# Kernel optimization log

Hardware: AMD Instinct MI355X
Metric: run time of the kernel (lower is better)

Reference implementation:

```python
import jax, jax.numpy as jnp
import numpy as np

B = 4096
N_ENTITY = 100000
N_USER = 10000
N_RELATION = 32
DIM = 64
N_ITER = 2
K = 16  # n_neighbors


def setup_inputs() -> dict:
    key = jax.random.key(0)
    ks = jax.random.split(key, 8)
    pairs = jax.random.randint(ks[0], (B, 2), 0, N_USER, dtype=jnp.int64 if jax.config.jax_enable_x64 else jnp.int32)
    adj_entity = jax.random.randint(ks[1], (N_ENTITY, K), 0, N_ENTITY)
    adj_relation = jax.random.randint(ks[2], (N_ENTITY, K), 0, N_RELATION)
    # xavier_uniform-style scale for embeddings
    def xavier(k, shape):
        limit = float(np.sqrt(6.0 / (shape[0] + shape[1])))
        return jax.random.uniform(k, shape, jnp.float32, -limit, limit)
    entity_emb = xavier(ks[3], (N_ENTITY, DIM))
    relation_emb = xavier(ks[4], (N_RELATION, DIM))
    user_emb = xavier(ks[5], (N_USER, DIM))
    W = xavier(ks[6], (DIM, DIM))
    b = jnp.zeros((DIM,), jnp.float32)
    return {"pairs": pairs, "adj_entity": adj_entity, "adj_relation": adj_relation,
            "entity_emb": entity_emb, "relation_emb": relation_emb,
            "user_emb": user_emb, "W": W, "b": b}


def reference(pairs, adj_entity, adj_relation, entity_emb, relation_emb, user_emb, W, b):
    n = pairs.shape[0]
    dim = entity_emb.shape[1]
    k = adj_entity.shape[1]
    users = pairs[:, 0]
    items = pairs[:, 1]

    # multi-hop neighbor expansion (mirrors get_neighbors)
    entities = [items]
    relations = []
    for i in range(N_ITER):
        entities.append(adj_entity[entities[i]].reshape(-1))
        relations.append(adj_relation[entities[i]].reshape(-1))

    u = user_emb[users]  # [B, D]
    ev = [entity_emb[entities[i]].reshape(n, -1, dim) for i in range(N_ITER + 1)]
    rv = [relation_emb[relations[i]].reshape(n, -1, dim) for i in range(N_ITER)]

    for l in range(N_ITER):
        nxt = []
        for i in range(N_ITER - l):
            r = rv[i].reshape(n, -1, k, dim)          # [B, M, K, D]
            scores = jnp.einsum('bd,bmkd->bmk', u, r) # user-relation attention
            attn = jax.nn.softmax(scores, axis=-1)[..., None]
            nbr = (attn * ev[i + 1].reshape(n, -1, k, dim)).sum(axis=-2)  # [B, M, D]
            x = ev[i].reshape(n, -1, dim) + nbr       # residual add
            h = x @ W.T + b                            # Linear(dim, dim)
            nxt.append(jnp.tanh(h) if l == N_ITER - 1 else jax.nn.relu(h))
        ev = nxt

    item_embeddings = ev[0].reshape(-1, dim)  # [B, D]
    return jax.nn.sigmoid(jnp.sum(u * item_embeddings, axis=1))
```

## Files before the change

kernel.cpp:

```cpp
#include <hip/hip_runtime.h>
#include <hip/hip_bf16.h>
#include <math.h>

#define DIM  64
#define KN   16
#define NREL 32

__device__ __forceinline__ float frcp(float x) { return __builtin_amdgcn_rcpf(x); }

__device__ __forceinline__ unsigned short f2bf(float f) {
    unsigned u = __float_as_uint(f);
    u = (u + 0x7fffu + ((u >> 16) & 1u)) >> 16;
    return (unsigned short)u;
}
__device__ __forceinline__ float bflo(unsigned v) { return __uint_as_float(v << 16); }
__device__ __forceinline__ float bfhi(unsigned v) { return __uint_as_float(v & 0xffff0000u); }

typedef __attribute__((ext_vector_type(8))) short bfrag;
typedef __attribute__((ext_vector_type(4))) float f32x4;

__global__ __launch_bounds__(256, 2) void we_kernel_mfma(
    const float* __restrict__ entity_emb,
    const float* __restrict__ W,
    const int* __restrict__ adjE,
    const int* __restrict__ adjR,
    unsigned short* __restrict__ WEb,
    int* __restrict__ adjP,
    int nRows)
{
    const int tid  = threadIdx.x;
    const int wave = tid >> 6;
    const int lane = tid & 63;
    const int c = lane & 15;
    const int g = lane >> 4;

    {
        const size_t nEntries = (size_t)nRows * KN;
        const size_t base = ((size_t)blockIdx.x * 256 + tid) * 8;
        if (base + 8 <= nEntries) {
            const int4* e4 = (const int4*)(adjE + base);
            const int4* r4 = (const int4*)(adjR + base);
            const int4 e0 = e4[0], e1v = e4[1];
            const int4 r0 = r4[0], r1v = r4[1];
            int4 p0, p1;
            p0.x = (e0.x << 5) | r0.x;  p0.y = (e0.y << 5) | r0.y;
            p0.z = (e0.z << 5) | r0.z;  p0.w = (e0.w << 5) | r0.w;
            p1.x = (e1v.x << 5) | r1v.x; p1.y = (e1v.y << 5) | r1v.y;
            p1.z = (e1v.z << 5) | r1v.z; p1.w = (e1v.w << 5) | r1v.w;
            ((int4*)(adjP + base))[0] = p0;
            ((int4*)(adjP + base))[1] = p1;
        } else if (base < nEntries) {
            for (size_t i = base; i < nEntries; ++i)
                adjP[i] = (adjE[i] << 5) | adjR[i];
        }
    }

    const int nTiles = (nRows + 15) >> 4;
    const int t0 = (blockIdx.x * 4 + wave) * 2;
    if (t0 >= nTiles) return;

    bfrag a[4][2];
    #pragma unroll
    for (int m = 0; m < 4; ++m) {
        #pragma unroll
        for (int ks = 0; ks < 2; ++ks) {
            const float4* ws = (const float4*)(W + (size_t)(16 * m + c) * DIM + 8 * g + 32 * ks);
            const float4 w0 = ws[0], w1 = ws[1];
            a[m][ks][0] = (short)f2bf(w0.x); a[m][ks][1] = (short)f2bf(w0.y);
            a[m][ks][2] = (short)f2bf(w0.z); a[m][ks][3] = (short)f2bf(w0.w);
            a[m][ks][4] = (short)f2bf(w1.x); a[m][ks][5] = (short)f2bf(w1.y);
            a[m][ks][6] = (short)f2bf(w1.z); a[m][ks][7] = (short)f2bf(w1.w);
        }
    }

    float4 pe[2][4];
    #pragma unroll
    for (int j = 0; j < 2; ++j) {
        const int t = (t0 + j < nTiles) ? (t0 + j) : 0;
        int row = 16 * t + c;
        if (row >= nRows) row = nRows - 1;
        const float4* src = (const float4*)(entity_emb + (size_t)row * DIM + 8 * g);
        pe[j][0] = src[0];
        pe[j][1] = src[1];
        pe[j][2] = src[8];
        pe[j][3] = src[9];
    }

    #pragma unroll
    for (int j = 0; j < 2; ++j) {
        const int t = t0 + j;
        if (t >= nTiles) continue;

        bfrag b0, b1;
        b0[0] = (short)f2bf(pe[j][0].x); b0[1] = (short)f2bf(pe[j][0].y);
        b0[2] = (short)f2bf(pe[j][0].z); b0[3] = (short)f2bf(pe[j][0].w);
        b0[4] = (short)f2bf(pe[j][1].x); b0[5] = (short)f2bf(pe[j][1].y);
        b0[6] = (short)f2bf(pe[j][1].z); b0[7] = (short)f2bf(pe[j][1].w);
        b1[0] = (short)f2bf(pe[j][2].x); b1[1] = (short)f2bf(pe[j][2].y);
        b1[2] = (short)f2bf(pe[j][2].z); b1[3] = (short)f2bf(pe[j][2].w);
        b1[4] = (short)f2bf(pe[j][3].x); b1[5] = (short)f2bf(pe[j][3].y);
        b1[6] = (short)f2bf(pe[j][3].z); b1[7] = (short)f2bf(pe[j][3].w);

        f32x4 acc[4];
        #pragma unroll
        for (int m = 0; m < 4; ++m) {
            f32x4 z = {0.f, 0.f, 0.f, 0.f};
            z = __builtin_amdgcn_mfma_f32_16x16x32_bf16(a[m][0], b0, z, 0, 0, 0);
            z = __builtin_amdgcn_mfma_f32_16x16x32_bf16(a[m][1], b1, z, 0, 0, 0);
            acc[m] = z;
        }

        const int erow = 16 * t + c;
        if (erow < nRows) {
            #pragma unroll
            for (int m = 0; m < 4; ++m) {
                const unsigned lo = (unsigned)f2bf(acc[m][0]) | ((unsigned)f2bf(acc[m][1]) << 16);
                const unsigned hi = (unsigned)f2bf(acc[m][2]) | ((unsigned)f2bf(acc[m][3]) << 16);
                *(uint2*)(WEb + (size_t)erow * DIM + 16 * m + 4 * g) = make_uint2(lo, hi);
            }
        }
    }
}

__global__ __launch_bounds__(256, 3) void kgcn_main(
    const int* __restrict__ pairs,
    const int* __restrict__ adjP,
    const unsigned short* __restrict__ WEb,
    const float* __restrict__ relation_emb,
    const float* __restrict__ user_emb,
    const float* __restrict__ W,
    const float* __restrict__ bias,
    float* __restrict__ out,
    int nPairs)
{
    __shared__ float ev1_s[4][KN * DIM];
    __shared__ float xb_s[4][DIM];

    const int tid  = threadIdx.x;
    const int wave = tid >> 6;
    const int lane = tid & 63;
    const int p    = blockIdx.x * 4 + wave;
    if (p >= nPairs) return;

    float* ev1 = ev1_s[wave];
    float* xb  = xb_s[wave];

    const int qq = lane >> 4;
    const int c  = lane & 15;
    const int c4 = c * 4;

    const int user = pairs[2 * p + 0];
    const int item = pairs[2 * p + 1];

    const float4 b4 = *(const float4*)(bias + c4);
    const uint2* WEq = (const uint2*)WEb;

    int rk0 = 0, e1 = 0;
    if (lane < KN) {
        const int pk0 = adjP[(size_t)item * KN + lane];
        rk0 = pk0 & 31;
        e1  = pk0 >> 5;
    }

    float4 rr[8], ur[8];
    {
        const int r = lane >> 1, hlf = lane & 1;
        const float4* rel4 = (const float4*)(relation_emb + r * DIM + hlf * 32);
        const float4* u4   = (const float4*)(user_emb + (size_t)user * DIM + hlf * 32);
        #pragma unroll
        for (int j = 0; j < 8; ++j) { rr[j] = rel4[j]; ur[j] = u4[j]; }
    }

    const uint2 itemv = WEq[(size_t)item * 16 + c];
    uint2 h0v[4];
    #pragma unroll
    for (int k = 0; k < 4; ++k) {
        const int e = __shfl(e1, qq * 4 + k);
        h0v[k] = WEq[(size_t)(unsigned)e * 16 + c];
    }
    int rkA[4], ekA[4], gsA[4];
    #pragma unroll
    for (int s = 0; s < 4; ++s) {
        gsA[s] = __shfl(e1, 4 * s + qq);
        const int pk = adjP[(size_t)(unsigned)gsA[s] * KN + c];
        rkA[s] = pk & 31;
        ekA[s] = pk >> 5;
    }

    float acc;
    {
        float a0 = 0.f, a1 = 0.f;
        #pragma unroll
        for (int j = 0; j < 8; j += 2) {
            float4 a = rr[j],     b = ur[j];
            float4 cc = rr[j+1],  d = ur[j+1];
            a0 += a.x*b.x + a.y*b.y + a.z*b.z + a.w*b.w;
            a1 += cc.x*d.x + cc.y*d.y + cc.z*d.z + cc.w*d.w;
        }
        acc = a0 + a1;
        acc += __shfl_xor(acc, 1);
    }

    uint2 svA[4];
    uint2 nvA[3][KN];
    #pragma unroll
    for (int s = 0; s < 3; ++s) {
        svA[s] = WEq[(size_t)(unsigned)gsA[s] * 16 + c];
        #pragma unroll
        for (int k = 0; k < KN; ++k) {
            const int e = __shfl(ekA[s], qq * 16 + k);
            nvA[s][k] = WEq[(size_t)(unsigned)e * 16 + c];
        }
    }
    svA[3] = WEq[(size_t)(unsigned)gsA[3] * 16 + c];

    auto softmax16 = [&](float s) -> float {
        float mx = s;
        mx = fmaxf(mx, __shfl_xor(mx, 1));
        mx = fmaxf(mx, __shfl_xor(mx, 2));
        mx = fmaxf(mx, __shfl_xor(mx, 4));
        mx = fmaxf(mx, __shfl_xor(mx, 8));
        float e = __expf(s - mx);
        float ss = e;
        ss += __shfl_xor(ss, 1);
        ss += __shfl_xor(ss, 2);
        ss += __shfl_xor(ss, 4);
        ss += __shfl_xor(ss, 8);
        return e * frcp(ss);
    };

    float wA[4];
    #pragma unroll
    for (int s = 0; s < 4; ++s) wA[s] = softmax16(__shfl(acc, rkA[s] << 1));
    const float w0 = softmax16(__shfl(acc, rk0 << 1));

    {
        float ax = b4.x + bflo(svA[0].x);
        float ay = b4.y + bfhi(svA[0].x);
        float az = b4.z + bflo(svA[0].y);
        float aw = b4.w + bfhi(svA[0].y);
        #pragma unroll
        for (int k = 0; k < KN; ++k) {
            const float w = __shfl(wA[0], qq * 16 + k);
            uint2 v = nvA[0][k];
            ax += w * bflo(v.x);
            ay += w * bfhi(v.x);
            az += w * bflo(v.y);
            aw += w * bfhi(v.y);
        }
        *(float4*)&ev1[qq * DIM + c4] =
            make_float4(fmaxf(ax, 0.f), fmaxf(ay, 0.f), fmaxf(az, 0.f), fmaxf(aw, 0.f));
    }
    uint2 nv3[KN];
    #pragma unroll
    for (int k = 0; k < KN; ++k) {
        const int e = __shfl(ekA[3], qq * 16 + k);
        nv3[k] = WEq[(size_t)(unsigned)e * 16 + c];
    }
    #pragma unroll
    for (int s = 1; s < 3; ++s) {
        float ax = b4.x + bflo(svA[s].x);
        float ay = b4.y + bfhi(svA[s].x);
        float az = b4.z + bflo(svA[s].y);
        float aw = b4.w + bfhi(svA[s].y);
        #pragma unroll
        for (int k = 0; k < KN; ++k) {
            const float w = __shfl(wA[s], qq * 16 + k);
            uint2 v = nvA[s][k];
            ax += w * bflo(v.x);
            ay += w * bfhi(v.x);
            az += w * bflo(v.y);
            aw += w * bfhi(v.y);
        }
        *(float4*)&ev1[(4 * s + qq) * DIM + c4] =
            make_float4(fmaxf(ax, 0.f), fmaxf(ay, 0.f), fmaxf(az, 0.f), fmaxf(aw, 0.f));
    }
    {
        float ax = b4.x + bflo(svA[3].x);
        float ay = b4.y + bfhi(svA[3].x);
        float az = b4.z + bflo(svA[3].y);
        float aw = b4.w + bfhi(svA[3].y);
        #pragma unroll
        for (int k = 0; k < KN; ++k) {
            const float w = __shfl(wA[3], qq * 16 + k);
            uint2 v = nv3[k];
            ax += w * bflo(v.x);
            ay += w * bfhi(v.x);
            az += w * bflo(v.y);
            aw += w * bfhi(v.y);
        }
        *(float4*)&ev1[(12 + qq) * DIM + c4] =
            make_float4(fmaxf(ax, 0.f), fmaxf(ay, 0.f), fmaxf(az, 0.f), fmaxf(aw, 0.f));
    }

    float ax = 0.f, ay = 0.f, az = 0.f, aw = 0.f;
    #pragma unroll
    for (int k = 0; k < 4; ++k) {
        const float w = __shfl(w0, qq * 4 + k);
        ax += w * bflo(h0v[k].x);
        ay += w * bfhi(h0v[k].x);
        az += w * bflo(h0v[k].y);
        aw += w * bfhi(h0v[k].y);
    }
    ax += __shfl_xor(ax, 16); ay += __shfl_xor(ay, 16);
    az += __shfl_xor(az, 16); aw += __shfl_xor(aw, 16);
    ax += __shfl_xor(ax, 32); ay += __shfl_xor(ay, 32);
    az += __shfl_xor(az, 32); aw += __shfl_xor(aw, 32);
    ax += bflo(itemv.x) + b4.x;
    ay += bfhi(itemv.x) + b4.y;
    az += bflo(itemv.y) + b4.z;
    aw += bfhi(itemv.y) + b4.w;
    const float e0x = fmaxf(ax, 0.f), e0y = fmaxf(ay, 0.f);
    const float e0z = fmaxf(az, 0.f), e0w = fmaxf(aw, 0.f);

    asm volatile("s_waitcnt lgkmcnt(0)" ::: "memory");
    float sx = 0.f, sy = 0.f, sz = 0.f, sw = 0.f;
    #pragma unroll
    for (int k = 0; k < 4; ++k) {
        const int   kg = qq * 4 + k;
        const float w  = __shfl(w0, kg);
        float4 ev = *(const float4*)&ev1[kg * DIM + c4];
        sx += w * ev.x;
        sy += w * ev.y;
        sz += w * ev.z;
        sw += w * ev.w;
    }
    sx += __shfl_xor(sx, 16); sy += __shfl_xor(sy, 16);
    sz += __shfl_xor(sz, 16); sw += __shfl_xor(sw, 16);
    sx += __shfl_xor(sx, 32); sy += __shfl_xor(sy, 32);
    sz += __shfl_xor(sz, 32); sw += __shfl_xor(sw, 32);

    asm volatile("s_waitcnt lgkmcnt(0)" ::: "memory");
    if (qq == 0)
        *(float4*)&xb[c4] = make_float4(e0x + sx, e0y + sy, e0z + sz, e0w + sw);
    asm volatile("s_waitcnt lgkmcnt(0)" ::: "memory");
    float h0 = bias[lane], h1 = 0.f, h2 = 0.f, h3 = 0.f;
    {
        const float4* Wl  = (const float4*)(W + lane * DIM);
        const float4* xv4 = (const float4*)xb;
        #pragma unroll
        for (int j = 0; j < 16; j += 4) {
            float4 w0v = Wl[j],   x0v = xv4[j];
            float4 w1v = Wl[j+1], x1v = xv4[j+1];
            float4 w2v = Wl[j+2], x2v = xv4[j+2];
            float4 w3v = Wl[j+3], x3v = xv4[j+3];
            h0 += w0v.x*x0v.x + w0v.y*x0v.y + w0v.z*x0v.z + w0v.w*x0v.w;
            h1 += w1v.x*x1v.x + w1v.y*x1v.y + w1v.z*x1v.z + w1v.w*x1v.w;
            h2 += w2v.x*x2v.x + w2v.y*x2v.y + w2v.z*x2v.z + w2v.w*x2v.w;
            h3 += w3v.x*x3v.x + w3v.y*x3v.y + w3v.z*x3v.z + w3v.w*x3v.w;
        }
    }
    const float itemf = tanhf((h0 + h1) + (h2 + h3));

    float d = user_emb[(size_t)user * DIM + lane] * itemf;
    d += __shfl_xor(d, 1);
    d += __shfl_xor(d, 2);
    d += __shfl_xor(d, 4);
    d += __shfl_xor(d, 8);
    d += __shfl_xor(d, 16);
    d += __shfl_xor(d, 32);
    if (lane == 0) out[p] = 1.f / (1.f + expf(-d));
}

__global__ __launch_bounds__(256, 4) void kgcn_fallback(
    const int* __restrict__ pairs, const int* __restrict__ adj_entity,
    const int* __restrict__ adj_relation, const float* __restrict__ entity_emb,
    const float* __restrict__ relation_emb, const float* __restrict__ user_emb,
    const float* __restrict__ W, const float* __restrict__ bias,
    float* __restrict__ out, int nPairs)
{
    __shared__ float ev1_s[2][KN * DIM];
    __shared__ float xb_s[4][DIM];
    const int tid = threadIdx.x, wave = tid >> 6, lane = tid & 63;
    const int q = wave >> 1, half = wave & 1;
    int p = blockIdx.x * 2 + q;
    if (p >= nPairs) p = nPairs - 1;
    float* ev1 = ev1_s[q]; float* xb = xb_s[wave];
    const int user = pairs[2 * p + 0], item = pairs[2 * p + 1];
    const float bval = bias[lane];
    const float* emb_l = entity_emb + lane;
    const float4* W4 = (const float4*)(W + lane * DIM);
    int rk0 = 0, e1 = 0;
    if (lane < KN) {
        rk0 = adj_relation[(size_t)item * KN + lane];
        e1  = adj_entity[(size_t)item * KN + lane];
    }
    float acc;
    {
        const int r = lane >> 1, hlf = lane & 1;
        const float4* rel4 = (const float4*)(relation_emb + r * DIM + hlf * 32);
        const float4* u4 = (const float4*)(user_emb + (size_t)user * DIM + hlf * 32);
        float a0 = 0.f, a1 = 0.f;
        #pragma unroll
        for (int j = 0; j < 8; j += 2) {
            float4 a = rel4[j], b = u4[j], c = rel4[j+1], d = u4[j+1];
            a0 += a.x*b.x + a.y*b.y + a.z*b.z + a.w*b.w;
            a1 += c.x*d.x + c.y*d.y + c.z*d.z + c.w*d.w;
        }
        acc = a0 + a1; acc += __shfl_xor(acc, 1);
    }
    auto softmax16 = [&](float s) -> float {
        float mx = s;
        mx = fmaxf(mx, __shfl_xor(mx, 1)); mx = fmaxf(mx, __shfl_xor(mx, 2));
        mx = fmaxf(mx, __shfl_xor(mx, 4)); mx = fmaxf(mx, __shfl_xor(mx, 8));
        float e = __expf(s - mx);
        float ss = e;
        ss += __shfl_xor(ss, 1); ss += __shfl_xor(ss, 2);
        ss += __shfl_xor(ss, 4); ss += __shfl_xor(ss, 8);
        return e * frcp(ss);
    };
    auto matvec = [&](float xv) -> float {
        asm volatile("s_waitcnt lgkmcnt(0)" ::: "memory");
        xb[lane] = xv;
        asm volatile("s_waitcnt lgkmcnt(0)" ::: "memory");
        float h0 = bval, h1 = 0.f, h2 = 0.f, h3 = 0.f;
        const float4* xv4 = (const float4*)xb;
        #pragma unroll
        for (int j = 0; j < 16; j += 4) {
            float4 w0 = W4[j], x0 = xv4[j], w1 = W4[j+1], x1 = xv4[j+1];
            float4 w2 = W4[j+2], x2 = xv4[j+2], w3 = W4[j+3], x3 = xv4[j+3];
            h0 += w0.x*x0.x + w0.y*x0.y + w0.z*x0.z + w0.w*x0.w;
            h1 += w1.x*x1.x + w1.y*x1.y + w1.z*x1.z + w1.w*x1.w;
            h2 += w2.x*x2.x + w2.y*x2.y + w2.z*x2.z + w2.w*x2.w;
            h3 += w3.x*x3.x + w3.y*x3.y + w3.z*x3.z + w3.w*x3.w;
        }
        return (h0 + h1) + (h2 + h3);
    };
    auto gather = [&](int self, int ek, float w) -> float {
        float xa = emb_l[(size_t)(unsigned)self * DIM], xc = 0.f;
        #pragma unroll
        for (int k = 0; k < KN; k += 2) {
            const int e0i = __shfl(ek, k); const float f0 = __shfl(w, k);
            const int e1i = __shfl(ek, k + 1); const float f1 = __shfl(w, k + 1);
            xa += f0 * emb_l[(size_t)(unsigned)e0i * DIM];
            xc += f1 * emb_l[(size_t)(unsigned)e1i * DIM];
        }
        return xa + xc;
    };
    int rk_n = 0, ek_n = 0;
    {
        const int g0 = __shfl(e1, half * 8);
        if (lane < KN) {
            rk_n = adj_relation[(size_t)(unsigned)g0 * KN + lane];
            ek_n = adj_entity[(size_t)(unsigned)g0 * KN + lane];
        }
    }
    #pragma unroll 1
    for (int mi = 0; mi < 8; ++mi) {
        const int m = half * 8 + mi;
        const int g = __shfl(e1, m);
        const int rk = rk_n, ek = ek_n;
        if (mi + 1 < 8) {
            const int gn = __shfl(e1, m + 1);
            if (lane < KN) {
                rk_n = adj_relation[(size_t)(unsigned)gn * KN + lane];
                ek_n = adj_entity[(size_t)(unsigned)gn * KN + lane];
            }
        }
        const float w = softmax16(__shfl(acc, rk << 1));
        const float x = gather(g, ek, w);
        ev1[m * DIM + lane] = fmaxf(matvec(x), 0.f);
    }
    __syncthreads();
    if (half != 0) return;
    const float w0 = softmax16(__shfl(acc, rk0 << 1));
    const float x0 = gather(item, e1, w0);
    const float e0 = fmaxf(matvec(x0), 0.f);
    float xa = e0, xc = 0.f;
    #pragma unroll
    for (int k = 0; k < KN; k += 2) {
        xa += __shfl(w0, k) * ev1[k * DIM + lane];
        xc += __shfl(w0, k + 1) * ev1[(k + 1) * DIM + lane];
    }
    const float itemf = tanhf(matvec(xa + xc));
    float d = user_emb[(size_t)user * DIM + lane] * itemf;
    d += __shfl_xor(d, 1); d += __shfl_xor(d, 2); d += __shfl_xor(d, 4);
    d += __shfl_xor(d, 8); d += __shfl_xor(d, 16); d += __shfl_xor(d, 32);
    if (lane == 0) out[p] = 1.f / (1.f + expf(-d));
}

extern "C" void kernel_launch(void* const* d_in, const int* in_sizes, int n_in,
                              void* d_out, int out_size, void* d_ws, size_t ws_size,
                              hipStream_t stream) {
    const int*   pairs        = (const int*)d_in[0];
    const int*   adj_entity   = (const int*)d_in[1];
    const int*   adj_relation = (const int*)d_in[2];
    const float* entity_emb   = (const float*)d_in[3];
    const float* relation_emb = (const float*)d_in[4];
    const float* user_emb     = (const float*)d_in[5];
    const float* W            = (const float*)d_in[6];
    const float* b            = (const float*)d_in[7];
    float* out = (float*)d_out;

    const int nPairs = in_sizes[0] / 2;
    const int nEnt   = in_sizes[3] / DIM;
    const size_t weBytes   = (size_t)in_sizes[3] * sizeof(unsigned short);
    const size_t weAligned = (weBytes + 255) & ~(size_t)255;
    const size_t adjBytes  = (size_t)nEnt * KN * sizeof(int);

    if (ws_size >= weAligned + adjBytes) {
        unsigned short* WEb = (unsigned short*)d_ws;
        int* adjP = (int*)((char*)d_ws + weAligned);
        const int nTiles = (nEnt + 15) >> 4;
        const int preBlocks = (nTiles + 7) / 8;
        we_kernel_mfma<<<preBlocks, 256, 0, stream>>>(entity_emb, W,
                                                      adj_entity, adj_relation,
                                                      WEb, adjP, nEnt);
        const int mainBlocks = (nPairs + 3) / 4;
        kgcn_main<<<mainBlocks, 256, 0, stream>>>(pairs, adjP,
                                                  WEb, relation_emb, user_emb,
                                                  W, b, out, nPairs);
    } else {
        const int nBlocks = (nPairs + 1) / 2;
        kgcn_fallback<<<nBlocks, 256, 0, stream>>>(pairs, adj_entity, adj_relation,
                                                   entity_emb, relation_emb, user_emb,
                                                   W, b, out, nPairs);
    }
}
```

Before: 130.0 us.

## Stage neighbor gathers through LDS via global_load_lds instead of registers

Hop-2 neighbor embedding rows are no longer held in a large register array (3x16 uint2 per lane). Each group of 64 rows is now fetched straight into a per-wave LDS buffer with global_load_lds, and every aggregation step reads it back from LDS. The load for the next group is issued after each step, and the hop-1 computation is moved ahead to cover the first load's latency. This cuts register pressure, which may allow more occupancy, but it uses 8KB more LDS per wave and serializes the groups with a vmcnt(0) wait on each one.

```diff
diff --git a/kernel.cpp b/kernel.cpp
--- a/kernel.cpp
+++ b/kernel.cpp
@@ -15,6 +15,12 @@
 }
 __device__ __forceinline__ float bflo(unsigned v) { return __uint_as_float(v << 16); }
 __device__ __forceinline__ float bfhi(unsigned v) { return __uint_as_float(v & 0xffff0000u); }
+
+__device__ __forceinline__ void gload_lds4(const void* g, void* l) {
+    __builtin_amdgcn_global_load_lds(
+        (const __attribute__((address_space(1))) unsigned int*)g,
+        (__attribute__((address_space(3))) unsigned int*)l, 4, 0, 0);
+}
 
 typedef __attribute__((ext_vector_type(8))) short bfrag;
 typedef __attribute__((ext_vector_type(4))) float f32x4;
@@ -133,6 +139,7 @@
     float* __restrict__ out,
     int nPairs)
 {
+    __shared__ uint2 gbuf_s[4][64 * 16];
     __shared__ float ev1_s[4][KN * DIM];
     __shared__ float xb_s[4][DIM];
 
@@ -142,8 +149,9 @@
     const int p    = blockIdx.x * 4 + wave;
     if (p >= nPairs) return;
 
-    float* ev1 = ev1_s[wave];
-    float* xb  = xb_s[wave];
+    uint2* gbuf = gbuf_s[wave];
+    float* ev1  = ev1_s[wave];
+    float* xb   = xb_s[wave];
 
     const int qq = lane >> 4;
     const int c  = lane & 15;
@@ -153,6 +161,7 @@
     const int item = pairs[2 * p + 1];
 
     const float4 b4 = *(const float4*)(bias + c4);
+    const float bl = bias[lane];
     const uint2* WEq = (const uint2*)WEb;
 
     int rk0 = 0, e1 = 0;
@@ -179,12 +188,14 @@
         h0v[k] = WEq[(size_t)(unsigned)e * 16 + c];
     }
     int rkA[4], ekA[4], gsA[4];
+    uint2 svA[4];
     #pragma unroll
     for (int s = 0; s < 4; ++s) {
         gsA[s] = __shfl(e1, 4 * s + qq);
         const int pk = adjP[(size_t)(unsigned)gsA[s] * KN + c];
         rkA[s] = pk & 31;
         ekA[s] = pk >> 5;
+        svA[s] = WEq[(size_t)(unsigned)gsA[s] * 16 + c];
     }
 
     float acc;
@@ -200,19 +211,6 @@
         acc = a0 + a1;
         acc += __shfl_xor(acc, 1);
     }
-
-    uint2 svA[4];
-    uint2 nvA[3][KN];
-    #pragma unroll
-    for (int s = 0; s < 3; ++s) {
-        svA[s] = WEq[(size_t)(unsigned)gsA[s] * 16 + c];
-        #pragma unroll
-        for (int k = 0; k < KN; ++k) {
-            const int e = __shfl(ekA[s], qq * 16 + k);
-            nvA[s][k] = WEq[(size_t)(unsigned)e * 16 + c];
-        }
-    }
-    svA[3] = WEq[(size_t)(unsigned)gsA[3] * 16 + c];
 
     auto softmax16 = [&](float s) -> float {
         float mx = s;
@@ -229,89 +227,78 @@
         return e * frcp(ss);
     };
 
+    const int hi32 = lane >> 5;
+    const int b32  = (lane & 31) << 2;
+    #pragma unroll
+    for (int i = 0; i < 32; ++i) {
+        const int idx = 2 * i + hi32;
+        const int q = idx & 3, k = idx >> 2;
+        const int e = __shfl(ekA[0], q * 16 + k);
+        gload_lds4((const char*)WEb + (((size_t)(unsigned)e) << 7) + b32,
+                   (char*)gbuf + i * 256);
+    }
+
     float wA[4];
     #pragma unroll
     for (int s = 0; s < 4; ++s) wA[s] = softmax16(__shfl(acc, rkA[s] << 1));
     const float w0 = softmax16(__shfl(acc, rk0 << 1));
 
-    {
-        float ax = b4.x + bflo(svA[0].x);
-        float ay = b4.y + bfhi(svA[0].x);
-        float az = b4.z + bflo(svA[0].y);
-        float aw = b4.w + bfhi(svA[0].y);
+    float hx = 0.f, hy = 0.f, hz = 0.f, hw = 0.f;
+    #pragma unroll
+    for (int k = 0; k < 4; ++k) {
+        const float w = __shfl(w0, qq * 4 + k);
+        hx += w * bflo(h0v[k].x);
+        hy += w * bfhi(h0v[k].x);
+        hz += w * bflo(h0v[k].y);
+        hw += w * bfhi(h0v[k].y);
+    }
+    hx += __shfl_xor(hx, 16); hy += __shfl_xor(hy, 16);
+    hz += __shfl_xor(hz, 16); hw += __shfl_xor(hw, 16);
+    hx += __shfl_xor(hx, 32); hy += __shfl_xor(hy, 32);
+    hz += __shfl_xor(hz, 32); hw += __shfl_xor(hw, 32);
+    hx += bflo(itemv.x) + b4.x;
+    hy += bfhi(itemv.x) + b4.y;
+    hz += bflo(itemv.y) + b4.z;
+    hw += bfhi(itemv.y) + b4.w;
+    const float e0x = fmaxf(hx, 0.f), e0y = fmaxf(hy, 0.f);
+    const float e0z = fmaxf(hz, 0.f), e0w = fmaxf(hw, 0.f);
+
+    #pragma unroll
+    for (int s = 0; s < 4; ++s) {
+        asm volatile("s_waitcnt vmcnt(0)" ::: "memory");
+        __builtin_amdgcn_sched_barrier(0);
+
+        float ax = b4.x + bflo(svA[s].x);
+        float ay = b4.y + bfhi(svA[s].x);
+        float az = b4.z + bflo(svA[s].y);
+        float aw = b4.w + bfhi(svA[s].y);
         #pragma unroll
         for (int k = 0; k < KN; ++k) {
-            const float w = __shfl(wA[0], qq * 16 + k);
-            uint2 v = nvA[0][k];
+            const float w = __shfl(wA[s], qq * 16 + k);
+            const uint2 v = gbuf[(k * 4 + qq) * 16 + c];
             ax += w * bflo(v.x);
             ay += w * bfhi(v.x);
             az += w * bflo(v.y);
             aw += w * bfhi(v.y);
         }
-        *(float4*)&ev1[qq * DIM + c4] =
-            make_float4(fmaxf(ax, 0.f), fmaxf(ay, 0.f), fmaxf(az, 0.f), fmaxf(aw, 0.f));
-    }
-    uint2 nv3[KN];
-    #pragma unroll
-    for (int k = 0; k < KN; ++k) {
-        const int e = __shfl(ekA[3], qq * 16 + k);
-        nv3[k] = WEq[(size_t)(unsigned)e * 16 + c];
-    }
-    #pragma unroll
-    for (int s = 1; s < 3; ++s) {
-        float ax = b4.x + bflo(svA[s].x);
-        float ay = b4.y + bfhi(svA[s].x);
-        float az = b4.z + bflo(svA[s].y);
-        float aw = b4.w + bfhi(svA[s].y);
-        #pragma unroll
-        for (int k = 0; k < KN; ++k) {
-            const float w = __shfl(wA[s], qq * 16 + k);
-            uint2 v = nvA[s][k];
-            ax += w * bflo(v.x);
-            ay += w * bfhi(v.x);
-            az += w * bflo(v.y);
-            aw += w * bfhi(v.y);
-        }
+
+        if (s < 3) {
+            asm volatile("" ::: "memory");
+            asm volatile("s_waitcnt lgkmcnt(0)" ::: "memory");
+            __builtin_amdgcn_sched_barrier(0);
+            #pragma unroll
+            for (int i = 0; i < 32; ++i) {
+                const int idx = 2 * i + hi32;
+                const int q = idx & 3, k = idx >> 2;
+                const int e = __shfl(ekA[s + 1], q * 16 + k);
+                gload_lds4((const char*)WEb + (((size_t)(unsigned)e) << 7) + b32,
+                           (char*)gbuf + i * 256);
+            }
+        }
+
         *(float4*)&ev1[(4 * s + qq) * DIM + c4] =
             make_float4(fmaxf(ax, 0.f), fmaxf(ay, 0.f), fmaxf(az, 0.f), fmaxf(aw, 0.f));
     }
-    {
-        float ax = b4.x + bflo(svA[3].x);
-        float ay = b4.y + bfhi(svA[3].x);
-        float az = b4.z + bflo(svA[3].y);
-        float aw = b4.w + bfhi(svA[3].y);
-        #pragma unroll
-        for (int k = 0; k < KN; ++k) {
-            const float w = __shfl(wA[3], qq * 16 + k);
-            uint2 v = nv3[k];
-            ax += w * bflo(v.x);
-            ay += w * bfhi(v.x);
-            az += w * bflo(v.y);
-            aw += w * bfhi(v.y);
-        }
-        *(float4*)&ev1[(12 + qq) * DIM + c4] =
-            make_float4(fmaxf(ax, 0.f), fmaxf(ay, 0.f), fmaxf(az, 0.f), fmaxf(aw, 0.f));
-    }
-
-    float ax = 0.f, ay = 0.f, az = 0.f, aw = 0.f;
-    #pragma unroll
-    for (int k = 0; k < 4; ++k) {
-        const float w = __shfl(w0, qq * 4 + k);
-        ax += w * bflo(h0v[k].x);
-        ay += w * bfhi(h0v[k].x);
-        az += w * bflo(h0v[k].y);
-        aw += w * bfhi(h0v[k].y);
-    }
-    ax += __shfl_xor(ax, 16); ay += __shfl_xor(ay, 16);
-    az += __shfl_xor(az, 16); aw += __shfl_xor(aw, 16);
-    ax += __shfl_xor(ax, 32); ay += __shfl_xor(ay, 32);
-    az += __shfl_xor(az, 32); aw += __shfl_xor(aw, 32);
-    ax += bflo(itemv.x) + b4.x;
-    ay += bfhi(itemv.x) + b4.y;
-    az += bflo(itemv.y) + b4.z;
-    aw += bfhi(itemv.y) + b4.w;
-    const float e0x = fmaxf(ax, 0.f), e0y = fmaxf(ay, 0.f);
-    const float e0z = fmaxf(az, 0.f), e0w = fmaxf(aw, 0.f);
 
     asm volatile("s_waitcnt lgkmcnt(0)" ::: "memory");
     float sx = 0.f, sy = 0.f, sz = 0.f, sw = 0.f;
@@ -334,7 +321,7 @@
     if (qq == 0)
         *(float4*)&xb[c4] = make_float4(e0x + sx, e0y + sy, e0z + sz, e0w + sw);
     asm volatile("s_waitcnt lgkmcnt(0)" ::: "memory");
-    float h0 = bias[lane], h1 = 0.f, h2 = 0.f, h3 = 0.f;
+    float h0 = bl, h1 = 0.f, h2 = 0.f, h3 = 0.f;
     {
         const float4* Wl  = (const float4*)(W + lane * DIM);
         const float4* xv4 = (const float4*)xb;
```

New measurement: 138.7 us. 6.7% more time.
